# Kernel tuning notes

Measured on AMD Instinct MI355X. Metric: run time of the kernel, lower is better.

## Reference

```python
import jax, jax.numpy as jnp
import numpy as np

OFFSET = 1  # self.offset

def setup_inputs() -> dict:
    key = jax.random.key(0)
    k1, k2, k3, k4, k5 = jax.random.split(key, 5)
    B, D, T, S, N = 16, 512, 1024, 12, 10
    x = jax.random.normal(k1, (B, D, T), dtype=jnp.float32)
    y = jax.random.normal(k2, (B, D, T), dtype=jnp.float32)
    W = jax.random.normal(k3, (D, D, S), dtype=jnp.float32) * 0.05  # ConvTranspose2d weight [in, out, 1, steps] squeezed
    b = jax.random.normal(k4, (D,), dtype=jnp.float32) * 0.05
    neg_idxs = jax.random.randint(k5, (B, N * T), 0, T)
    return {"x": x, "y": y, "W": W, "b": b, "neg_idxs": neg_idxs}


def reference(x, y, W, b, neg_idxs):
    B, F, T = y.shape
    N = neg_idxs.shape[1] // T
    # --- sample_negatives: gather by computed index over flattened y ---
    y_flat = jnp.transpose(y, (1, 0, 2)).reshape(F, B * T)          # [F, B*T]
    idx = (neg_idxs + jnp.arange(B, dtype=neg_idxs.dtype)[:, None] * T).reshape(-1)
    negs = y_flat[:, idx].reshape(F, B, N, T).transpose(2, 1, 0, 3)  # [N, B, F, T]
    targets = jnp.concatenate([y[None], negs], axis=0)               # [C=N+1, B, F, T]
    # --- project_to_steps: ConvTranspose2d with kernel (1, steps) == per-step linear ---
    xp = jnp.einsum('bit,ios->bots', x, W) + b[None, :, None, None]  # [B, F, T, S]
    C = N + 1
    S = xp.shape[-1]
    steps = min(S, T - OFFSET)
    preds, labels = [], []
    for i in range(steps):  # small fixed loop over prediction steps
        off = i + OFFSET
        # [C, B, T-off]: dot over feature dim, copies broadcast over x
        p = jnp.einsum('bft,cbft->cbt', xp[:, :, :T - off, i], targets[:, :, :, off:])
        preds.append(p.reshape(-1))
        lab = jnp.zeros((C, B * (T - off)), dtype=xp.dtype).at[0].set(1.0)
        labels.append(lab.reshape(-1))
    predictions = jnp.concatenate(preds)
    labels_out = jnp.concatenate(labels)
    return predictions, labels_out
```

## Files before the change

kernel.cpp:

```cpp
#include <hip/hip_runtime.h>

typedef __bf16 bf16x8 __attribute__((ext_vector_type(8)));
typedef float f32x4 __attribute__((ext_vector_type(4)));

#define B_ 16
#define T_ 1024
#define D_ 512
#define S_ 12
#define C_ 11
static constexpr int P_TOTAL = 2148960;

__device__ __host__ inline constexpr int pred_base(int i) {
  return C_ * B_ * (T_ * i - (i * (i + 1)) / 2);
}

__device__ inline unsigned short f2bf(float f) {
  unsigned int u = __float_as_uint(f);
  u += 0x7FFF + ((u >> 16) & 1);
  return (unsigned short)(u >> 16);
}

__device__ inline void gld16(const void* g, void* l) {
  __builtin_amdgcn_global_load_lds(
      (const __attribute__((address_space(1))) void*)g,
      (__attribute__((address_space(3))) void*)l, 16, 0, 0);
}

__global__ __launch_bounds__(256) void prep_w(const float* __restrict__ W,
                                              unsigned short* __restrict__ wt) {
  __shared__ unsigned short tile[32][33][12];
  const int i0 = blockIdx.x * 32, o0 = blockIdx.y * 32;
#pragma unroll
  for (int q = 0; q < 48; ++q) {
    int idx = threadIdx.x + q * 256;
    int ii = idx / 384, rem = idx % 384;
    tile[ii][rem / 12][rem % 12] =
        f2bf(W[(size_t)(i0 + ii) * 6144 + (size_t)o0 * 12 + rem]);
  }
  __syncthreads();
#pragma unroll
  for (int q = 0; q < 48; ++q) {
    int idx = threadIdx.x + q * 256;
    int ss = idx / 1024, rem = idx % 1024;
    int oo = rem / 32, ii = rem % 32;
    wt[(size_t)ss * (D_ * D_) + (size_t)(o0 + oo) * D_ + (i0 + ii)] = tile[ii][oo][ss];
  }
}

__global__ __launch_bounds__(256) void prep_t(const float* __restrict__ in,
                                              unsigned short* __restrict__ ob) {
  __shared__ float tile[32][33];
  const int t0 = blockIdx.x * 32;
  const int d0 = blockIdx.y * 32;
  const int b = blockIdx.z;
  const float* ib = in + (size_t)b * D_ * T_;
  const int r = threadIdx.x / 32, c = threadIdx.x % 32;
#pragma unroll
  for (int p = 0; p < 4; ++p) {
    int rr = r + p * 8;
    tile[rr][c] = ib[(size_t)(d0 + rr) * T_ + t0 + c];
  }
  __syncthreads();
  unsigned short* op = ob + (size_t)b * T_ * D_;
#pragma unroll
  for (int p = 0; p < 4; ++p) {
    int rr = r + p * 8;
    op[(size_t)(t0 + rr) * D_ + d0 + c] = f2bf(tile[c][rr]);
  }
}

__global__ void labels_k(float* __restrict__ lab) {
  int k = blockIdx.x * 256 + threadIdx.x;
  if (k >= P_TOTAL) return;
  int i = 0;
#pragma unroll
  for (int q = 1; q < 12; ++q)
    if (k >= pred_base(q)) i = q;
  int rel = k - pred_base(i);
  int len = T_ - 1 - i;
  lab[k] = (rel < B_ * len) ? 1.0f : 0.0f;
}

__global__ __launch_bounds__(512, 2) void gemm_xp(
    const unsigned short* __restrict__ xb,
    const unsigned short* __restrict__ wt,
    const float* __restrict__ bias,
    unsigned short* __restrict__ xp,
    int m0_global) {
  __shared__ unsigned short lds[65536];
  const int tid = threadIdx.x;
  const int s = blockIdx.z;
  const int n0 = blockIdx.y * 256;
  const int ml0 = blockIdx.x * 256;
  const unsigned short* Ag = xb + (size_t)(m0_global + ml0) * D_;
  const unsigned short* Bg = wt + ((size_t)s * D_ + n0) * D_;

  auto stage = [&](const unsigned short* src, int kt, int regionShorts) {
#pragma unroll
    for (int h = 0; h < 2; ++h) {
      int o = tid * 16 + h * 8192;
      int row = o >> 6;
      int sc = (o >> 4) & 3;
      int lcol = (sc ^ ((row >> 1) & 3)) << 4;
      gld16((const char*)src + (size_t)row * (D_ * 2) + kt * 64 + lcol,
            (char*)&lds[regionShorts] + o);
    }
  };

  const int w = tid >> 6, l = tid & 63;
  const int gm = w >> 2, gn = w & 3;
  const int fr = l & 15, sgrp = l >> 4;

  auto rdfrag = [&](const unsigned short* base, int row) -> bf16x8 {
    int idx = row * 32 + ((sgrp ^ ((row >> 1) & 3)) << 3);
    return *(const bf16x8*)&base[idx];
  };

  f32x4 acc[2][4][4];
#pragma unroll
  for (int ms = 0; ms < 2; ++ms)
#pragma unroll
    for (int fm = 0; fm < 4; ++fm)
#pragma unroll
      for (int fn = 0; fn < 4; ++fn)
#pragma unroll
        for (int e = 0; e < 4; ++e) acc[ms][fm][fn][e] = 0.f;

  stage(Ag, 0, 0);
  stage(Bg, 0, 8192);
  stage(Ag, 1, 16384);
  stage(Bg, 1, 16384 + 8192);
  asm volatile("s_waitcnt vmcnt(4)" ::: "memory");
  __builtin_amdgcn_s_barrier();

  for (int kt = 0; kt < 16; ++kt) {
    const unsigned short* A_l = &lds[(kt & 3) * 16384];
    const unsigned short* B_l = A_l + 8192;
    bf16x8 afrag[4], bfrag[4];

#pragma unroll
    for (int fn = 0; fn < 4; ++fn)
      bfrag[fn] = rdfrag(B_l, gn * 64 + fn * 16 + fr);
#pragma unroll
    for (int fm = 0; fm < 4; ++fm)
      afrag[fm] = rdfrag(A_l, gm * 128 + fm * 16 + fr);
    if (kt + 2 < 16) stage(Ag, kt + 2, ((kt + 2) & 3) * 16384);
    __builtin_amdgcn_s_barrier();
    __builtin_amdgcn_s_setprio(1);
#pragma unroll
    for (int fm = 0; fm < 4; ++fm)
#pragma unroll
      for (int fn = 0; fn < 4; ++fn)
        acc[0][fm][fn] = __builtin_amdgcn_mfma_f32_16x16x32_bf16(
            afrag[fm], bfrag[fn], acc[0][fm][fn], 0, 0, 0);
    __builtin_amdgcn_s_setprio(0);
    __builtin_amdgcn_s_barrier();

#pragma unroll
    for (int fm = 0; fm < 4; ++fm)
      afrag[fm] = rdfrag(A_l, gm * 128 + 64 + fm * 16 + fr);
    if (kt + 2 < 16) stage(Bg, kt + 2, ((kt + 2) & 3) * 16384 + 8192);
    __builtin_amdgcn_s_barrier();
    __builtin_amdgcn_s_setprio(1);
#pragma unroll
    for (int fm = 0; fm < 4; ++fm)
#pragma unroll
      for (int fn = 0; fn < 4; ++fn)
        acc[1][fm][fn] = __builtin_amdgcn_mfma_f32_16x16x32_bf16(
            afrag[fm], bfrag[fn], acc[1][fm][fn], 0, 0, 0);
    __builtin_amdgcn_s_setprio(0);
    if (kt <= 13) {
      asm volatile("s_waitcnt vmcnt(4)" ::: "memory");
    } else if (kt == 14) {
      asm volatile("s_waitcnt vmcnt(0)" ::: "memory");
    }
    __builtin_amdgcn_s_barrier();
  }

  float bv[4];
#pragma unroll
  for (int fn = 0; fn < 4; ++fn) bv[fn] = bias[n0 + gn * 64 + fn * 16 + fr];

#pragma unroll
  for (int ms = 0; ms < 2; ++ms) {
#pragma unroll
    for (int fm = 0; fm < 4; ++fm) {
#pragma unroll
      for (int r = 0; r < 4; ++r) {
        int m = ml0 + gm * 128 + ms * 64 + fm * 16 + (l >> 4) * 4 + r;
        int bl = m >> 10, t = m & 1023;
        size_t orow = (((size_t)bl * S_ + s) * T_ + t) * D_;
#pragma unroll
        for (int fn = 0; fn < 4; ++fn) {
          int o = n0 + gn * 64 + fn * 16 + fr;
          xp[orow + o] = f2bf(acc[ms][fm][fn][r] + bv[fn]);
        }
      }
    }
  }
}

__global__ __launch_bounds__(256) void pred_k(
    const unsigned short* __restrict__ xp,
    const unsigned short* __restrict__ yT,
    const int* __restrict__ negs,
    float* __restrict__ preds, int b0) {
  const int w = threadIdx.x >> 6, l = threadIdx.x & 63;
  const int tt = blockIdx.x * 4 + w;
  const int bl = blockIdx.y;
  const int b = b0 + bl;
  if (tt < 1 || tt >= T_) return;

  const int fr = l & 15;
  const int koff = (l >> 4) * 8;

  int t = tt - 1 - fr;
  bool av = (fr < S_) && (t >= 0);
  int si = av ? fr : 0;
  int st = av ? t : 0;
  const unsigned short* arow = xp + (((size_t)bl * S_ + si) * T_ + st) * D_;

  int j = tt;
  if (fr >= 1 && fr <= 10) j = negs[b * (10 * T_) + (fr - 1) * T_ + tt];
  const unsigned short* brow = yT + ((size_t)b * T_ + j) * D_;

  f32x4 acc;
#pragma unroll
  for (int e = 0; e < 4; ++e) acc[e] = 0.f;
#pragma unroll
  for (int kk = 0; kk < 16; ++kk) {
    bf16x8 a = *(const bf16x8*)(arow + kk * 32 + koff);
    bf16x8 bb = *(const bf16x8*)(brow + kk * 32 + koff);
    acc = __builtin_amdgcn_mfma_f32_16x16x32_bf16(a, bb, acc, 0, 0, 0);
  }
#pragma unroll
  for (int r = 0; r < 4; ++r) {
    int ii = (l >> 4) * 4 + r;
    int to = tt - 1 - ii;
    if (ii < S_ && fr < C_ && to >= 0) {
      int len = T_ - 1 - ii;
      preds[pred_base(ii) + ((size_t)fr * B_ + b) * len + to] = acc[r];
    }
  }
}

extern "C" void kernel_launch(void* const* d_in, const int* in_sizes, int n_in,
                              void* d_out, int out_size, void* d_ws, size_t ws_size,
                              hipStream_t stream) {
  (void)in_sizes; (void)n_in; (void)out_size;
  const float* x = (const float*)d_in[0];
  const float* y = (const float*)d_in[1];
  const float* W = (const float*)d_in[2];
  const float* bias = (const float*)d_in[3];
  const int* negs = (const int*)d_in[4];
  float* out = (float*)d_out;
  char* ws = (char*)d_ws;

  unsigned short* wt = (unsigned short*)ws;
  unsigned short* xb = (unsigned short*)(ws + 6291456);
  unsigned short* yT = (unsigned short*)(ws + 6291456 + 16777216);
  unsigned short* xp = (unsigned short*)(ws + 6291456 + 2 * 16777216);
  const size_t fixed = 6291456 + (size_t)2 * 16777216;
  const size_t xp_per_b = (size_t)S_ * T_ * D_ * 2;
  int nb = 1;
  if (ws_size > fixed) {
    size_t cap = (ws_size - fixed) / xp_per_b;
    nb = cap < 1 ? 1 : (cap > 16 ? 16 : (int)cap);
  }

  hipLaunchKernelGGL(prep_w, dim3(16, 16), dim3(256), 0, stream, W, wt);
  hipLaunchKernelGGL(prep_t, dim3(32, 16, 16), dim3(256), 0, stream, x, xb);
  hipLaunchKernelGGL(prep_t, dim3(32, 16, 16), dim3(256), 0, stream, y, yT);
  hipLaunchKernelGGL(labels_k, dim3((P_TOTAL + 255) / 256), dim3(256), 0, stream,
                     out + P_TOTAL);

  for (int b0 = 0; b0 < B_; b0 += nb) {
    int bc = (B_ - b0) < nb ? (B_ - b0) : nb;
    hipLaunchKernelGGL(gemm_xp, dim3(bc * 4, 2, 12), dim3(512), 0, stream,
                       xb, wt, bias, xp, b0 * T_);
    hipLaunchKernelGGL(pred_k, dim3(256, bc), dim3(256), 0, stream,
                       xp, yT, negs, out, b0);
  }
}
```

Before: 223.4 us.

## Make GEMM persistent with cross-tile prefetch, merge prep launches, double pred work

The projection GEMM becomes a persistent kernel with a grid capped at 256 blocks. Each block loops over tiles and prefetches the next tile's first K-slices during the tail of the current one, which hides the pipeline fill and drain between tiles. The two transpose/convert launches for x and y are merged into one launch, and each pred_k wave now computes two time positions so more loads are in flight. These add persistent-loop bookkeeping and register pressure. They also remove a barrier per iteration, which makes correctness of the LDS slot reuse depend on the remaining waitcnt/barrier ordering.

```diff
diff --git a/kernel.cpp b/kernel.cpp
--- a/kernel.cpp
+++ b/kernel.cpp
@@ -47,12 +47,16 @@
   }
 }
 
-__global__ __launch_bounds__(256) void prep_t(const float* __restrict__ in,
-                                              unsigned short* __restrict__ ob) {
+__global__ __launch_bounds__(256) void prep_t2(const float* __restrict__ xin,
+                                               const float* __restrict__ yin,
+                                               unsigned short* __restrict__ xo,
+                                               unsigned short* __restrict__ yo) {
   __shared__ float tile[32][33];
   const int t0 = blockIdx.x * 32;
   const int d0 = blockIdx.y * 32;
-  const int b = blockIdx.z;
+  const int b = blockIdx.z & 15;
+  const float* in = (blockIdx.z < 16) ? xin : yin;
+  unsigned short* ob = (blockIdx.z < 16) ? xo : yo;
   const float* ib = in + (size_t)b * D_ * T_;
   const int r = threadIdx.x / 32, c = threadIdx.x % 32;
 #pragma unroll
@@ -86,117 +90,147 @@
     const unsigned short* __restrict__ wt,
     const float* __restrict__ bias,
     unsigned short* __restrict__ xp,
-    int m0_global) {
+    int m0_global, int tiles, int mtiles) {
   __shared__ unsigned short lds[65536];
   const int tid = threadIdx.x;
-  const int s = blockIdx.z;
-  const int n0 = blockIdx.y * 256;
-  const int ml0 = blockIdx.x * 256;
-  const unsigned short* Ag = xb + (size_t)(m0_global + ml0) * D_;
-  const unsigned short* Bg = wt + ((size_t)s * D_ + n0) * D_;
-
-  auto stage = [&](const unsigned short* src, int kt, int regionShorts) {
-#pragma unroll
-    for (int h = 0; h < 2; ++h) {
-      int o = tid * 16 + h * 8192;
-      int row = o >> 6;
-      int sc = (o >> 4) & 3;
-      int lcol = (sc ^ ((row >> 1) & 3)) << 4;
-      gld16((const char*)src + (size_t)row * (D_ * 2) + kt * 64 + lcol,
-            (char*)&lds[regionShorts] + o);
-    }
-  };
-
   const int w = tid >> 6, l = tid & 63;
   const int gm = w >> 2, gn = w & 3;
   const int fr = l & 15, sgrp = l >> 4;
+
+  const int so0 = tid * 16;
+  const int row0 = so0 >> 6, sc0 = (so0 >> 4) & 3;
+  const int go0 = row0 * 1024 + ((sc0 ^ ((row0 >> 1) & 3)) << 4);
+  const int so1 = so0 + 8192;
+  const int row1 = so1 >> 6, sc1 = (so1 >> 4) & 3;
+  const int go1 = row1 * 1024 + ((sc1 ^ ((row1 >> 1) & 3)) << 4);
+
+  auto stage = [&](const unsigned short* srcKt, int slotShorts) {
+    gld16((const char*)srcKt + go0, (char*)&lds[slotShorts] + so0);
+    gld16((const char*)srcKt + go1, (char*)&lds[slotShorts] + so1);
+  };
 
   auto rdfrag = [&](const unsigned short* base, int row) -> bf16x8 {
     int idx = row * 32 + ((sgrp ^ ((row >> 1) & 3)) << 3);
     return *(const bf16x8*)&base[idx];
   };
 
-  f32x4 acc[2][4][4];
-#pragma unroll
-  for (int ms = 0; ms < 2; ++ms)
-#pragma unroll
-    for (int fm = 0; fm < 4; ++fm)
-#pragma unroll
-      for (int fn = 0; fn < 4; ++fn)
-#pragma unroll
-        for (int e = 0; e < 4; ++e) acc[ms][fm][fn][e] = 0.f;
-
-  stage(Ag, 0, 0);
-  stage(Bg, 0, 8192);
-  stage(Ag, 1, 16384);
-  stage(Bg, 1, 16384 + 8192);
+  auto decode = [&](int t, const unsigned short*& Ag, const unsigned short*& Bg,
+                    int& n0v, int& miv, int& siv) {
+    miv = t % mtiles;
+    int rest = t / mtiles;
+    int ni = rest & 1;
+    siv = rest >> 1;
+    Ag = xb + (size_t)(miv * 256) * D_;
+    Bg = wt + ((size_t)siv * D_ + ni * 256) * D_;
+    n0v = ni * 256;
+  };
+  (void)m0_global;
+
+  int ti = blockIdx.x;
+  if (ti >= tiles) return;
+  const unsigned short *Ag, *Bg, *Agn = nullptr, *Bgn = nullptr;
+  int n0, mi, si, n0n, min_, sin_;
+  decode(ti, Ag, Bg, n0, mi, si);
+  int tin = ti + gridDim.x;
+  bool hasNext = tin < tiles;
+  if (hasNext) decode(tin, Agn, Bgn, n0n, min_, sin_);
+
+  stage(Ag, 0);
+  stage(Bg, 8192);
+  stage(Ag + 32, 16384);
+  stage(Bg + 32, 16384 + 8192);
   asm volatile("s_waitcnt vmcnt(4)" ::: "memory");
   __builtin_amdgcn_s_barrier();
 
-  for (int kt = 0; kt < 16; ++kt) {
-    const unsigned short* A_l = &lds[(kt & 3) * 16384];
-    const unsigned short* B_l = A_l + 8192;
-    bf16x8 afrag[4], bfrag[4];
-
-#pragma unroll
-    for (int fn = 0; fn < 4; ++fn)
-      bfrag[fn] = rdfrag(B_l, gn * 64 + fn * 16 + fr);
-#pragma unroll
-    for (int fm = 0; fm < 4; ++fm)
-      afrag[fm] = rdfrag(A_l, gm * 128 + fm * 16 + fr);
-    if (kt + 2 < 16) stage(Ag, kt + 2, ((kt + 2) & 3) * 16384);
-    __builtin_amdgcn_s_barrier();
-    __builtin_amdgcn_s_setprio(1);
-#pragma unroll
-    for (int fm = 0; fm < 4; ++fm)
+  while (true) {
+    f32x4 acc[2][4][4];
+#pragma unroll
+    for (int ms = 0; ms < 2; ++ms)
+#pragma unroll
+      for (int fm = 0; fm < 4; ++fm)
+#pragma unroll
+        for (int fn = 0; fn < 4; ++fn)
+#pragma unroll
+          for (int e = 0; e < 4; ++e) acc[ms][fm][fn][e] = 0.f;
+
+    float bv[4];
+#pragma unroll
+    for (int fn = 0; fn < 4; ++fn) bv[fn] = bias[n0 + gn * 64 + fn * 16 + fr];
+
+    for (int kt = 0; kt < 16; ++kt) {
+      const int sl = kt & 3;
+      const unsigned short* A_l = &lds[sl * 16384];
+      const unsigned short* B_l = A_l + 8192;
+      const int k2 = kt + 2;
+      const int sl2s = (k2 & 3) * 16384;
+      const unsigned short* sA = nullptr;
+      const unsigned short* sB = nullptr;
+      if (k2 < 16) {
+        sA = Ag + k2 * 32;
+        sB = Bg + k2 * 32;
+      } else if (hasNext) {
+        sA = Agn + (k2 - 16) * 32;
+        sB = Bgn + (k2 - 16) * 32;
+      }
+      bf16x8 af[4], bfr[4];
+
 #pragma unroll
       for (int fn = 0; fn < 4; ++fn)
-        acc[0][fm][fn] = __builtin_amdgcn_mfma_f32_16x16x32_bf16(
-            afrag[fm], bfrag[fn], acc[0][fm][fn], 0, 0, 0);
-    __builtin_amdgcn_s_setprio(0);
-    __builtin_amdgcn_s_barrier();
-
-#pragma unroll
-    for (int fm = 0; fm < 4; ++fm)
-      afrag[fm] = rdfrag(A_l, gm * 128 + 64 + fm * 16 + fr);
-    if (kt + 2 < 16) stage(Bg, kt + 2, ((kt + 2) & 3) * 16384 + 8192);
-    __builtin_amdgcn_s_barrier();
-    __builtin_amdgcn_s_setprio(1);
-#pragma unroll
-    for (int fm = 0; fm < 4; ++fm)
-#pragma unroll
-      for (int fn = 0; fn < 4; ++fn)
-        acc[1][fm][fn] = __builtin_amdgcn_mfma_f32_16x16x32_bf16(
-            afrag[fm], bfrag[fn], acc[1][fm][fn], 0, 0, 0);
-    __builtin_amdgcn_s_setprio(0);
-    if (kt <= 13) {
+        bfr[fn] = rdfrag(B_l, gn * 64 + fn * 16 + fr);
+#pragma unroll
+      for (int fm = 0; fm < 4; ++fm)
+        af[fm] = rdfrag(A_l, gm * 128 + fm * 16 + fr);
+      if (sA) stage(sA, sl2s);
+      __builtin_amdgcn_s_barrier();
+      __builtin_amdgcn_s_setprio(1);
+#pragma unroll
+      for (int fm = 0; fm < 4; ++fm)
+#pragma unroll
+        for (int fn = 0; fn < 4; ++fn)
+          acc[0][fm][fn] = __builtin_amdgcn_mfma_f32_16x16x32_bf16(
+              af[fm], bfr[fn], acc[0][fm][fn], 0, 0, 0);
+      __builtin_amdgcn_s_setprio(0);
+
+#pragma unroll
+      for (int fm = 0; fm < 4; ++fm)
+        af[fm] = rdfrag(A_l, gm * 128 + 64 + fm * 16 + fr);
+      if (sB) stage(sB, sl2s + 8192);
       asm volatile("s_waitcnt vmcnt(4)" ::: "memory");
-    } else if (kt == 14) {
-      asm volatile("s_waitcnt vmcnt(0)" ::: "memory");
+      __builtin_amdgcn_s_barrier();
+      __builtin_amdgcn_s_setprio(1);
+#pragma unroll
+      for (int fm = 0; fm < 4; ++fm)
+#pragma unroll
+        for (int fn = 0; fn < 4; ++fn)
+          acc[1][fm][fn] = __builtin_amdgcn_mfma_f32_16x16x32_bf16(
+              af[fm], bfr[fn], acc[1][fm][fn], 0, 0, 0);
+      __builtin_amdgcn_s_setprio(0);
     }
-    __builtin_amdgcn_s_barrier();
-  }
-
-  float bv[4];
-#pragma unroll
-  for (int fn = 0; fn < 4; ++fn) bv[fn] = bias[n0 + gn * 64 + fn * 16 + fr];
-
-#pragma unroll
-  for (int ms = 0; ms < 2; ++ms) {
-#pragma unroll
-    for (int fm = 0; fm < 4; ++fm) {
-#pragma unroll
-      for (int r = 0; r < 4; ++r) {
-        int m = ml0 + gm * 128 + ms * 64 + fm * 16 + (l >> 4) * 4 + r;
-        int bl = m >> 10, t = m & 1023;
-        size_t orow = (((size_t)bl * S_ + s) * T_ + t) * D_;
-#pragma unroll
-        for (int fn = 0; fn < 4; ++fn) {
-          int o = n0 + gn * 64 + fn * 16 + fr;
-          xp[orow + o] = f2bf(acc[ms][fm][fn][r] + bv[fn]);
+
+#pragma unroll
+    for (int ms = 0; ms < 2; ++ms) {
+#pragma unroll
+      for (int fm = 0; fm < 4; ++fm) {
+#pragma unroll
+        for (int r = 0; r < 4; ++r) {
+          int m = mi * 256 + gm * 128 + ms * 64 + fm * 16 + sgrp * 4 + r;
+          int bl = m >> 10, t = m & 1023;
+          size_t orow = (((size_t)bl * S_ + si) * T_ + t) * D_;
+#pragma unroll
+          for (int fn = 0; fn < 4; ++fn) {
+            int o = n0 + gn * 64 + fn * 16 + fr;
+            xp[orow + o] = f2bf(acc[ms][fm][fn][r] + bv[fn]);
+          }
         }
       }
     }
+
+    if (!hasNext) break;
+    ti = tin;
+    Ag = Agn; Bg = Bgn; n0 = n0n; mi = min_; si = sin_;
+    tin = ti + gridDim.x;
+    hasNext = tin < tiles;
+    if (hasNext) decode(tin, Agn, Bgn, n0n, min_, sin_);
   }
 }
 
@@ -206,40 +240,53 @@
     const int* __restrict__ negs,
     float* __restrict__ preds, int b0) {
   const int w = threadIdx.x >> 6, l = threadIdx.x & 63;
-  const int tt = blockIdx.x * 4 + w;
   const int bl = blockIdx.y;
   const int b = b0 + bl;
-  if (tt < 1 || tt >= T_) return;
-
   const int fr = l & 15;
   const int koff = (l >> 4) * 8;
-
-  int t = tt - 1 - fr;
-  bool av = (fr < S_) && (t >= 0);
-  int si = av ? fr : 0;
-  int st = av ? t : 0;
-  const unsigned short* arow = xp + (((size_t)bl * S_ + si) * T_ + st) * D_;
-
-  int j = tt;
-  if (fr >= 1 && fr <= 10) j = negs[b * (10 * T_) + (fr - 1) * T_ + tt];
-  const unsigned short* brow = yT + ((size_t)b * T_ + j) * D_;
-
-  f32x4 acc;
-#pragma unroll
-  for (int e = 0; e < 4; ++e) acc[e] = 0.f;
+  const int tta = blockIdx.x * 4 + w;
+  const int ttb = tta + 512;
+
+  int ta = tta - 1 - fr;
+  bool ava = (fr < S_) && (ta >= 0);
+  const unsigned short* arowA =
+      xp + (((size_t)bl * S_ + (ava ? fr : 0)) * T_ + (ava ? ta : 0)) * D_;
+  int tb = ttb - 1 - fr;
+  bool avb = (fr < S_) && (tb >= 0);
+  const unsigned short* arowB =
+      xp + (((size_t)bl * S_ + (avb ? fr : 0)) * T_ + (avb ? tb : 0)) * D_;
+
+  int ja = tta, jb = ttb;
+  if (fr >= 1 && fr <= 10) {
+    ja = negs[b * (10 * T_) + (fr - 1) * T_ + tta];
+    jb = negs[b * (10 * T_) + (fr - 1) * T_ + ttb];
+  }
+  const unsigned short* browA = yT + ((size_t)b * T_ + ja) * D_;
+  const unsigned short* browB = yT + ((size_t)b * T_ + jb) * D_;
+
+  f32x4 accA, accB;
+#pragma unroll
+  for (int e = 0; e < 4; ++e) { accA[e] = 0.f; accB[e] = 0.f; }
 #pragma unroll
   for (int kk = 0; kk < 16; ++kk) {
-    bf16x8 a = *(const bf16x8*)(arow + kk * 32 + koff);
-    bf16x8 bb = *(const bf16x8*)(brow + kk * 32 + koff);
-    acc = __builtin_amdgcn_mfma_f32_16x16x32_bf16(a, bb, acc, 0, 0, 0);
+    bf16x8 a0 = *(const bf16x8*)(arowA + kk * 32 + koff);
+    bf16x8 b0v = *(const bf16x8*)(browA + kk * 32 + koff);
+    bf16x8 a1 = *(const bf16x8*)(arowB + kk * 32 + koff);
+    bf16x8 b1v = *(const bf16x8*)(browB + kk * 32 + koff);
+    accA = __builtin_amdgcn_mfma_f32_16x16x32_bf16(a0, b0v, accA, 0, 0, 0);
+    accB = __builtin_amdgcn_mfma_f32_16x16x32_bf16(a1, b1v, accB, 0, 0, 0);
   }
 #pragma unroll
   for (int r = 0; r < 4; ++r) {
     int ii = (l >> 4) * 4 + r;
-    int to = tt - 1 - ii;
-    if (ii < S_ && fr < C_ && to >= 0) {
+    if (ii < S_ && fr < C_) {
       int len = T_ - 1 - ii;
-      preds[pred_base(ii) + ((size_t)fr * B_ + b) * len + to] = acc[r];
+      int toa = tta - 1 - ii;
+      if (tta >= 1 && toa >= 0)
+        preds[pred_base(ii) + ((size_t)fr * B_ + b) * len + toa] = accA[r];
+      int tob = ttb - 1 - ii;
+      if (tob >= 0)
+        preds[pred_base(ii) + ((size_t)fr * B_ + b) * len + tob] = accB[r];
     }
   }
 }
@@ -269,16 +316,18 @@
   }
 
   hipLaunchKernelGGL(prep_w, dim3(16, 16), dim3(256), 0, stream, W, wt);
-  hipLaunchKernelGGL(prep_t, dim3(32, 16, 16), dim3(256), 0, stream, x, xb);
-  hipLaunchKernelGGL(prep_t, dim3(32, 16, 16), dim3(256), 0, stream, y, yT);
+  hipLaunchKernelGGL(prep_t2, dim3(32, 16, 32), dim3(256), 0, stream, x, y, xb, yT);
   hipLaunchKernelGGL(labels_k, dim3((P_TOTAL + 255) / 256), dim3(256), 0, stream,
                      out + P_TOTAL);
 
   for (int b0 = 0; b0 < B_; b0 += nb) {
     int bc = (B_ - b0) < nb ? (B_ - b0) : nb;
-    hipLaunchKernelGGL(gemm_xp, dim3(bc * 4, 2, 12), dim3(512), 0, stream,
-                       xb, wt, bias, xp, b0 * T_);
-    hipLaunchKernelGGL(pred_k, dim3(256, bc), dim3(256), 0, stream,
+    int tiles = bc * 4 * 2 * 12;
+    int grid = tiles < 256 ? tiles : 256;
+    hipLaunchKernelGGL(gemm_xp, dim3(grid), dim3(512), 0, stream,
+                       xb + (size_t)b0 * T_ * D_, wt, bias, xp, b0 * T_,
+                       tiles, bc * 4);
+    hipLaunchKernelGGL(pred_k, dim3(128, bc), dim3(256), 0, stream,
                        xp, yT, negs, out, b0);
   }
 }
```

Measured after the change: 216.3 us. -3.2%, faster.
